# Optimization experiments

Measured on AMD Instinct MI355X. Metric: run time of the kernel, lower is better.

The kernel has to match this reference:

```python
import jax, jax.numpy as jnp
import numpy as np

BIN = 48
CPG = BIN * 3            # 144 hidden channels
SCALE = 2.0 / (BIN - 1)  # quantization step


def _causal_mask(k, include_center):
    # PixelCNN-style raster causal mask for a k x k kernel
    m = np.zeros((k, k), np.float32)
    c = k // 2
    m[:c, :] = 1.0
    m[c, :c] = 1.0
    if include_center:
        m[c, c] = 1.0
    return jnp.asarray(m)

MASK_NC = _causal_mask(5, False)  # first layer: strictly causal (exclude center)
MASK_C = _causal_mask(5, True)    # hidden/final layers: include center


def mconv(x, w, b, mask):
    # masked 5x5 conv, SAME padding, NCHW / OIHW
    y = jax.lax.conv_general_dilated(x, w * mask, (1, 1), 'SAME',
                                     dimension_numbers=('NCHW', 'OIHW', 'NCHW'))
    return y + b[None, :, None, None]


def setup_inputs() -> dict:
    key = jax.random.key(0)
    ks = jax.random.split(key, 8)
    H, W = 256, 512
    std = 0.02
    # quantized code in [-1, 1] on the bin grid, as produced by the decode loop
    lv = jax.random.randint(ks[0], (1, 1, H, W), 0, BIN)
    x = lv.astype(jnp.float32) * SCALE - 1.0
    return {
        'x': x,
        'w0': jax.random.normal(ks[1], (CPG, 1, 5, 5), jnp.float32) * std,
        'b0': jax.random.normal(ks[2], (CPG,), jnp.float32) * std,
        'wr': jax.random.normal(ks[3], (10, CPG, CPG, 5, 5), jnp.float32) * std,
        'br': jax.random.normal(ks[4], (10, CPG), jnp.float32) * std,
        'wf': jax.random.normal(ks[5], (BIN + 1, CPG, 5, 5), jnp.float32) * std,
        'bf': jax.random.normal(ks[6], (BIN + 1,), jnp.float32) * std,
    }


def reference(x, w0, b0, wr, br, wf, bf):
    # causal conv entropy network (CconvDc stack + 5 residual blocks)
    h = jax.nn.relu(mconv(x, w0, b0, MASK_NC))
    for i in range(5):  # EntropyResidualBlockD x5 (fixed small layer loop)
        y = jax.nn.relu(mconv(h, wr[2 * i], br[2 * i], MASK_C))
        y = jax.nn.relu(mconv(y, wr[2 * i + 1], br[2 * i + 1], MASK_C))
        h = h + y
    logits = mconv(h, wf, bf, MASK_C)            # (1, BIN+1, H, W)
    probs = jax.nn.softmax(logits, axis=1)       # per-pixel symbol distribution (EntropyTable input)

    # tail of forward: importance code -> channel mask -> depth-to-space x2
    tcode = jnp.floor((x + 1.0) / SCALE + 1e-5)  # (1,1,H,W) in [0, BIN-1]
    ch = jnp.arange(BIN * 4, dtype=x.dtype)[None, :, None, None]
    tmask = (ch < tcode * 4.0).astype(x.dtype)   # Imp2mask: (1, 4*BIN, H, W)
    N, C, H, W = tmask.shape
    t = tmask.reshape(N, C // 4, 2, 2, H, W)
    t = t.transpose(0, 1, 4, 2, 5, 3).reshape(N, C // 4, 2 * H, 2 * W)  # Dtow(2)
    return probs, t
```

## Files before the change

### kernel.cpp

```cpp
#include <hip/hip_runtime.h>
#include <hip/hip_bf16.h>
#include <stdint.h>

#define H 256
#define W 512
#define NCG 18
#define AW 520
#define AH 258
#define XB 16
#define ROWB (AW*XB)
#define CGB (AH*ROWB)
#define ACTB ((size_t)NCG*(size_t)CGB)
#define KG 236
#define NCHUNK 59
#define CHUNKB 9216
#define WPH_B ((size_t)KG*144*16)
#define WPF_B ((size_t)KG*64*16)

typedef float f32x4 __attribute__((ext_vector_type(4)));
typedef short bf16x8 __attribute__((ext_vector_type(8)));

__device__ __forceinline__ float bf2f(unsigned short u) {
  union { unsigned int i; float f; } v; v.i = ((unsigned int)u) << 16; return v.f;
}
__device__ __forceinline__ unsigned short f2bf(float f) {
  __hip_bfloat16 h = __float2bfloat16(f);
  return __builtin_bit_cast(unsigned short, h);
}
__device__ __forceinline__ void gload_lds16(const void* g, void* l) {
  __builtin_amdgcn_global_load_lds(
      (const __attribute__((address_space(1))) unsigned int*)g,
      (__attribute__((address_space(3))) unsigned int*)l, 16, 0, 0);
}

__global__ void k_pack_h(const float* __restrict__ wr, char* __restrict__ wph) {
  int idx = blockIdx.x * 256 + threadIdx.x;
  if (idx >= 10 * 144 * 144) return;
  int ci = idx % 144; int rem = idx / 144; int co = rem % 144; int layer = rem / 144;
  const float* src = wr + (size_t)((layer * 144 + co) * 144 + ci) * 25;
  unsigned short* dstL = (unsigned short*)(wph + (size_t)layer * WPH_B);
  int cig = ci >> 3, cis = ci & 7;
#pragma unroll
  for (int tap = 0; tap < 13; ++tap) {
    int ky = (tap >= 5) + (tap >= 10);
    int kx = tap - ky * 5;
    dstL[((size_t)(tap * 18 + cig) * 144 + co) * 8 + cis] = f2bf(src[ky * 5 + kx]);
  }
}
__global__ void k_pack_f(const float* __restrict__ wf, char* __restrict__ wpf) {
  int idx = blockIdx.x * 256 + threadIdx.x;
  if (idx >= 49 * 144) return;
  int ci = idx % 144; int co = idx / 144;
  const float* src = wf + (size_t)(co * 144 + ci) * 25;
  unsigned short* dst = (unsigned short*)wpf;
  int cig = ci >> 3, cis = ci & 7;
#pragma unroll
  for (int tap = 0; tap < 13; ++tap) {
    int ky = (tap >= 5) + (tap >= 10);
    int kx = tap - ky * 5;
    dst[((size_t)(tap * 18 + cig) * 64 + co) * 8 + cis] = f2bf(src[ky * 5 + kx]);
  }
}
__global__ void k_biaspad(const float* __restrict__ bf, float* __restrict__ bfp) {
  int i = threadIdx.x;
  bfp[i] = (i < 49) ? bf[i] : -1e30f;
}

__global__ void k_layer0(const float* __restrict__ x, const float* __restrict__ w0,
                         const float* __restrict__ b0, char* __restrict__ act) {
  int i = blockIdx.x * 256 + threadIdx.x;
  int y = i >> 9, xx = i & 511;
  float xv[12];
#pragma unroll
  for (int tp = 0; tp < 12; ++tp) {
    int ky = (tp >= 5) + (tp >= 10);
    int kx = tp - ky * 5;
    int yy = y + ky - 2, xs = xx + kx - 2;
    bool ok = (yy >= 0) && (xs >= 0) && (xs < W);
    xv[tp] = ok ? x[yy * W + xs] : 0.f;
  }
  char* ob = act + (size_t)(y + 2) * ROWB + (size_t)(xx + 2) * XB;
  for (int cg = 0; cg < NCG; ++cg) {
    unsigned int us[4];
#pragma unroll
    for (int h2 = 0; h2 < 4; ++h2) {
      unsigned int lohi = 0;
#pragma unroll
      for (int p = 0; p < 2; ++p) {
        int co = cg * 8 + h2 * 2 + p;
        float a = b0[co];
#pragma unroll
        for (int tp = 0; tp < 12; ++tp) {
          int ky = (tp >= 5) + (tp >= 10);
          int kx = tp - ky * 5;
          a += w0[co * 25 + ky * 5 + kx] * xv[tp];
        }
        a = fmaxf(a, 0.f);
        lohi |= ((unsigned int)f2bf(a)) << (16 * p);
      }
      us[h2] = lohi;
    }
    uint4 v; v.x = us[0]; v.y = us[1]; v.z = us[2]; v.w = us[3];
    *(uint4*)(ob + (size_t)cg * CGB) = v;
  }
}

__global__ __launch_bounds__(256, 2)
void k_conv(const char* __restrict__ in, char* __restrict__ out,
            const char* __restrict__ wp, const float* __restrict__ bias, int res) {
  __shared__ __align__(16) char lA[2][CHUNKB];
  const int tid = threadIdx.x;
  const int wid = tid >> 6, lane = tid & 63;
  const int col = lane & 15, g = lane >> 4;

  int bid = blockIdx.x;
  int xcd = bid & 7, idx = bid >> 3;
  int by = xcd * 8 + (idx >> 3), bx = idx & 7;
  int y = by * 4 + wid, x0 = bx * 64;

  int pxo[4];
#pragma unroll
  for (int t = 0; t < 4; ++t) pxo[t] = (x0 + 16 * t + col) * XB;
  const char* bbase = in + (size_t)y * ROWB;

  f32x4 acc[9][4];
#pragma unroll
  for (int m = 0; m < 9; ++m)
#pragma unroll
    for (int t = 0; t < 4; ++t) acc[m][t] = (f32x4){0.f, 0.f, 0.f, 0.f};

  int ci = g << 3, tap = 0;
  bf16x8 bc[4], bn[4];

  {
    int off = (ci >> 3) * (int)CGB;
#pragma unroll
    for (int t = 0; t < 4; ++t) bc[t] = *(const bf16x8*)(bbase + (size_t)(off + pxo[t]));
  }
  ci += 32; if (ci >= 144) { ci -= 144; ++tap; }

#pragma unroll
  for (int j0 = 0; j0 < 3; ++j0) {
    int j = wid + j0 * 4;
    if (j < 9) gload_lds16(wp + (size_t)j * 1024 + (lane << 4), &lA[0][j * 1024]);
  }
  asm volatile("s_waitcnt vmcnt(0)" ::: "memory");
  __builtin_amdgcn_s_barrier();
  asm volatile("" ::: "memory");

#pragma unroll 1
  for (int c = 0; c < NCHUNK; ++c) {
    const char* ldsp = &lA[c & 1][0];
    if (c < NCHUNK - 1) {
      char* ldsn = &lA[(c & 1) ^ 1][0];
      const char* wsrc = wp + (size_t)(c + 1) * CHUNKB;
#pragma unroll
      for (int j0 = 0; j0 < 3; ++j0) {
        int j = wid + j0 * 4;
        if (j < 9) gload_lds16(wsrc + (size_t)j * 1024 + (lane << 4), ldsn + j * 1024);
      }
      asm volatile("" ::: "memory");
      int ky = (tap >= 5) + (tap >= 10);
      int kx = tap - ky * 5;
      int off = (ci >> 3) * (int)CGB + ky * (int)ROWB + (kx << 4);
#pragma unroll
      for (int t = 0; t < 4; ++t) bn[t] = *(const bf16x8*)(bbase + (size_t)(off + pxo[t]));
      ci += 32; if (ci >= 144) { ci -= 144; ++tap; }
      asm volatile("" ::: "memory");
    }
    const char* abase = ldsp + ((g * 144 + col) << 4);
#pragma unroll
    for (int m = 0; m < 9; ++m) {
      bf16x8 a = *(const bf16x8*)(abase + m * 256);
#pragma unroll
      for (int t = 0; t < 4; ++t)
        acc[m][t] = __builtin_amdgcn_mfma_f32_16x16x32_bf16(a, bc[t], acc[m][t], 0, 0, 0);
    }
    if (c < NCHUNK - 1) {
#pragma unroll
      for (int t = 0; t < 4; ++t) bc[t] = bn[t];
      asm volatile("s_waitcnt vmcnt(4)" ::: "memory");
      __builtin_amdgcn_s_barrier();
      asm volatile("" ::: "memory");
    }
  }

  const int sub = (g & 1) * 8;
#pragma unroll
  for (int m = 0; m < 9; ++m) {
    int co0 = m * 16 + (g << 2);
    f32x4 bv = *(const f32x4*)(bias + co0);
    char* ob = out + (size_t)(co0 >> 3) * CGB + (size_t)(y + 2) * ROWB + sub + 32;
#pragma unroll
    for (int t = 0; t < 4; ++t) {
      char* oa = ob + pxo[t];
      float v0 = fmaxf(acc[m][t][0] + bv[0], 0.f);
      float v1 = fmaxf(acc[m][t][1] + bv[1], 0.f);
      float v2 = fmaxf(acc[m][t][2] + bv[2], 0.f);
      float v3 = fmaxf(acc[m][t][3] + bv[3], 0.f);
      if (res) {
        uint2 old = *(const uint2*)oa;
        v0 += bf2f((unsigned short)(old.x & 0xffff));
        v1 += bf2f((unsigned short)(old.x >> 16));
        v2 += bf2f((unsigned short)(old.y & 0xffff));
        v3 += bf2f((unsigned short)(old.y >> 16));
      }
      uint2 st;
      st.x = (unsigned int)f2bf(v0) | ((unsigned int)f2bf(v1) << 16);
      st.y = (unsigned int)f2bf(v2) | ((unsigned int)f2bf(v3) << 16);
      *(uint2*)oa = st;
    }
  }
}

__global__ __launch_bounds__(256, 2)
void k_convf(const char* __restrict__ in, float* __restrict__ probs,
             const char* __restrict__ wp, const float* __restrict__ bfp) {
  __shared__ __align__(16) char lA[2][4096];
  const int tid = threadIdx.x;
  const int wid = tid >> 6, lane = tid & 63;
  const int col = lane & 15, g = lane >> 4;

  int bid = blockIdx.x;
  int xcd = bid & 7, idx = bid >> 3;
  int by = xcd * 8 + (idx >> 3), bx = idx & 7;
  int y = by * 4 + wid, x0 = bx * 64;

  int pxo[4];
#pragma unroll
  for (int t = 0; t < 4; ++t) pxo[t] = (x0 + 16 * t + col) * XB;
  const char* bbase = in + (size_t)y * ROWB;

  f32x4 acc[4][4];
#pragma unroll
  for (int m = 0; m < 4; ++m)
#pragma unroll
    for (int t = 0; t < 4; ++t) acc[m][t] = (f32x4){0.f, 0.f, 0.f, 0.f};

  int ci = g << 3, tap = 0;
  bf16x8 bc[4], bn[4];
  {
    int off = (ci >> 3) * (int)CGB;
#pragma unroll
    for (int t = 0; t < 4; ++t) bc[t] = *(const bf16x8*)(bbase + (size_t)(off + pxo[t]));
  }
  ci += 32; if (ci >= 144) { ci -= 144; ++tap; }

  if (wid < 4) gload_lds16(wp + (size_t)wid * 1024 + (lane << 4), &lA[0][wid * 1024]);
  asm volatile("s_waitcnt vmcnt(0)" ::: "memory");
  __builtin_amdgcn_s_barrier();
  asm volatile("" ::: "memory");

#pragma unroll 1
  for (int c = 0; c < NCHUNK; ++c) {
    const char* ldsp = &lA[c & 1][0];
    if (c < NCHUNK - 1) {
      char* ldsn = &lA[(c & 1) ^ 1][0];
      const char* wsrc = wp + (size_t)(c + 1) * 4096;
      if (wid < 4) gload_lds16(wsrc + (size_t)wid * 1024 + (lane << 4), ldsn + wid * 1024);
      asm volatile("" ::: "memory");
      int ky = (tap >= 5) + (tap >= 10);
      int kx = tap - ky * 5;
      int off = (ci >> 3) * (int)CGB + ky * (int)ROWB + (kx << 4);
#pragma unroll
      for (int t = 0; t < 4; ++t) bn[t] = *(const bf16x8*)(bbase + (size_t)(off + pxo[t]));
      ci += 32; if (ci >= 144) { ci -= 144; ++tap; }
      asm volatile("" ::: "memory");
    }
    const char* abase = ldsp + ((g * 64 + col) << 4);
#pragma unroll
    for (int m = 0; m < 4; ++m) {
      bf16x8 a = *(const bf16x8*)(abase + m * 256);
#pragma unroll
      for (int t = 0; t < 4; ++t)
        acc[m][t] = __builtin_amdgcn_mfma_f32_16x16x32_bf16(a, bc[t], acc[m][t], 0, 0, 0);
    }
    if (c < NCHUNK - 1) {
#pragma unroll
      for (int t = 0; t < 4; ++t) bc[t] = bn[t];
      asm volatile("s_waitcnt vmcnt(4)" ::: "memory");
      __builtin_amdgcn_s_barrier();
      asm volatile("" ::: "memory");
    }
  }

#pragma unroll
  for (int t = 0; t < 4; ++t) {
    float lg[4][4];
    float mx = -1e30f;
#pragma unroll
    for (int m = 0; m < 4; ++m) {
      f32x4 bv = *(const f32x4*)(bfp + m * 16 + (g << 2));
#pragma unroll
      for (int r = 0; r < 4; ++r) {
        lg[m][r] = acc[m][t][r] + bv[r];
        mx = fmaxf(mx, lg[m][r]);
      }
    }
    mx = fmaxf(mx, __shfl_xor(mx, 16));
    mx = fmaxf(mx, __shfl_xor(mx, 32));
    float s = 0.f;
#pragma unroll
    for (int m = 0; m < 4; ++m)
#pragma unroll
      for (int r = 0; r < 4; ++r) {
        lg[m][r] = __expf(lg[m][r] - mx);
        s += lg[m][r];
      }
    s += __shfl_xor(s, 16);
    s += __shfl_xor(s, 32);
    float inv = 1.f / s;
    int xp = x0 + 16 * t + col;
    float* op = probs + (size_t)y * W + xp;
#pragma unroll
    for (int m = 0; m < 4; ++m)
#pragma unroll
      for (int r = 0; r < 4; ++r) {
        int co = m * 16 + (g << 2) + r;
        if (co < 49) op[(size_t)co * (H * W)] = lg[m][r] * inv;
      }
  }
}

__global__ void k_tmask(const float* __restrict__ x, float* __restrict__ out1) {
  int i = blockIdx.x * 256 + threadIdx.x;
  int yy = i >> 10, xx = i & 1023;
  float xv = x[(yy >> 1) * W + (xx >> 1)];
  float tc = floorf((xv + 1.0f) / (float)(2.0 / 47.0) + 1e-5f);
#pragma unroll 4
  for (int g = 0; g < 48; ++g)
    out1[(size_t)g * (512 * 1024) + i] = ((float)g < tc) ? 1.0f : 0.0f;
}

extern "C" void kernel_launch(void* const* d_in, const int* in_sizes, int n_in,
                              void* d_out, int out_size, void* d_ws, size_t ws_size,
                              hipStream_t stream) {
  const float* x  = (const float*)d_in[0];
  const float* w0 = (const float*)d_in[1];
  const float* b0 = (const float*)d_in[2];
  const float* wr = (const float*)d_in[3];
  const float* br = (const float*)d_in[4];
  const float* wf = (const float*)d_in[5];
  const float* bf = (const float*)d_in[6];

  char* ws   = (char*)d_ws;
  char* actA = ws;
  char* actB = ws + ACTB;
  char* wph  = ws + 2 * ACTB;
  char* wpf  = wph + 10 * WPH_B;
  float* bfp = (float*)(wpf + WPF_B);
  size_t total = 2 * ACTB + 10 * WPH_B + WPF_B + 256;

  hipMemsetAsync(d_ws, 0, total, stream);

  k_pack_h<<<(10 * 144 * 144 + 255) / 256, 256, 0, stream>>>(wr, wph);
  k_pack_f<<<(49 * 144 + 255) / 256, 256, 0, stream>>>(wf, wpf);
  k_biaspad<<<1, 64, 0, stream>>>(bf, bfp);

  k_layer0<<<512, 256, 0, stream>>>(x, w0, b0, actA);

  for (int i = 0; i < 5; ++i) {
    k_conv<<<512, 256, 0, stream>>>(actA, actB, wph + (size_t)(2 * i) * WPH_B,
                                    br + (2 * i) * 144, 0);
    k_conv<<<512, 256, 0, stream>>>(actB, actA, wph + (size_t)(2 * i + 1) * WPH_B,
                                    br + (2 * i + 1) * 144, 1);
  }

  float* probs = (float*)d_out;
  k_convf<<<512, 256, 0, stream>>>(actA, probs, wpf, bfp);
  k_tmask<<<2048, 256, 0, stream>>>(x, probs + (size_t)49 * H * W);
}
```

Before: 902.5 us.

## Zero only activation halos, reorder K-chunks cig-major, unroll double-buffer loop

Replaces the full workspace memset, which cleared both large activation buffers, with a small kernel that zeroes only their padding borders; weights are still memset. Packed weight order changes from tap-major to channel-group-major so each chunk's four groups walk consecutive taps of the same channel group, which may improve cache locality of the activation reads. The main conv loops are unrolled by two with explicit ping-pong register and LDS buffers, removing the per-iteration register copy and conditionals. The risk is that interior halo assumptions are now correct only if every interior pixel is written before it is read.

```diff
diff --git a/kernel.cpp b/kernel.cpp
--- a/kernel.cpp
+++ b/kernel.cpp
@@ -44,7 +44,7 @@
   for (int tap = 0; tap < 13; ++tap) {
     int ky = (tap >= 5) + (tap >= 10);
     int kx = tap - ky * 5;
-    dstL[((size_t)(tap * 18 + cig) * 144 + co) * 8 + cis] = f2bf(src[ky * 5 + kx]);
+    dstL[((size_t)(cig * 13 + tap) * 144 + co) * 8 + cis] = f2bf(src[ky * 5 + kx]);
   }
 }
 __global__ void k_pack_f(const float* __restrict__ wf, char* __restrict__ wpf) {
@@ -58,12 +58,24 @@
   for (int tap = 0; tap < 13; ++tap) {
     int ky = (tap >= 5) + (tap >= 10);
     int kx = tap - ky * 5;
-    dst[((size_t)(tap * 18 + cig) * 64 + co) * 8 + cis] = f2bf(src[ky * 5 + kx]);
+    dst[((size_t)(cig * 13 + tap) * 64 + co) * 8 + cis] = f2bf(src[ky * 5 + kx]);
   }
 }
 __global__ void k_biaspad(const float* __restrict__ bf, float* __restrict__ bfp) {
   int i = threadIdx.x;
   bfp[i] = (i < 49) ? bf[i] : -1e30f;
+}
+
+__global__ void k_zeropad(char* __restrict__ actA, char* __restrict__ actB) {
+  int i = blockIdx.x * 256 + threadIdx.x;
+  if (i >= 2 * 18 * 2064) return;
+  int s = i % 2064; int p = i / 2064; int cig = p % 18; int buf = p / 18;
+  char* base = (buf ? actB : actA) + (size_t)cig * CGB;
+  int row, colpx;
+  if (s < 1040) { row = s / 520; colpx = s - row * 520; }
+  else { int s2 = s - 1040; row = 2 + (s2 >> 2); int m = s2 & 3; colpx = (m < 2) ? m : (512 + m); }
+  uint4 z; z.x = z.y = z.z = z.w = 0u;
+  *(uint4*)(base + (size_t)row * ROWB + (size_t)colpx * 16) = z;
 }
 
 __global__ void k_layer0(const float* __restrict__ x, const float* __restrict__ w0,
@@ -129,61 +141,64 @@
 #pragma unroll
     for (int t = 0; t < 4; ++t) acc[m][t] = (f32x4){0.f, 0.f, 0.f, 0.f};
 
-  int ci = g << 3, tap = 0;
-  bf16x8 bc[4], bn[4];
-
-  {
-    int off = (ci >> 3) * (int)CGB;
-#pragma unroll
-    for (int t = 0; t < 4; ++t) bc[t] = *(const bf16x8*)(bbase + (size_t)(off + pxo[t]));
-  }
-  ci += 32; if (ci >= 144) { ci -= 144; ++tap; }
-
-#pragma unroll
-  for (int j0 = 0; j0 < 3; ++j0) {
-    int j = wid + j0 * 4;
-    if (j < 9) gload_lds16(wp + (size_t)j * 1024 + (lane << 4), &lA[0][j * 1024]);
-  }
+  bf16x8 bA[4], bB[4];
+
+  auto bload = [&](bf16x8 (&dst)[4], int c) __attribute__((always_inline)) {
+    int kg = 4 * c + g;
+    if (kg >= 234) kg = 0;
+    int cig = kg / 13;
+    int tap = kg - cig * 13;
+    int ky = (tap >= 5) + (tap >= 10);
+    int kx = tap - ky * 5;
+    int off = cig * (int)CGB + ky * (int)ROWB + (kx << 4);
+#pragma unroll
+    for (int t = 0; t < 4; ++t) dst[t] = *(const bf16x8*)(bbase + (size_t)(off + pxo[t]));
+  };
+
+  auto stage = [&](char* ldsn, int c) __attribute__((always_inline)) {
+    const char* wsrc = wp + (size_t)c * CHUNKB;
+#pragma unroll
+    for (int j0 = 0; j0 < 3; ++j0) {
+      int j = wid + j0 * 4;
+      if (j < 9) gload_lds16(wsrc + (size_t)j * 1024 + (lane << 4), ldsn + j * 1024);
+    }
+  };
+
+  auto domfma = [&](const char* ldsc, bf16x8 (&bcur)[4]) __attribute__((always_inline)) {
+    const char* abase = ldsc + ((g * 144 + col) << 4);
+#pragma unroll
+    for (int m = 0; m < 9; ++m) {
+      bf16x8 a = *(const bf16x8*)(abase + m * 256);
+#pragma unroll
+      for (int t = 0; t < 4; ++t)
+        acc[m][t] = __builtin_amdgcn_mfma_f32_16x16x32_bf16(a, bcur[t], acc[m][t], 0, 0, 0);
+    }
+  };
+
+  auto phase = [&](const char* ldsc, char* ldsn, bf16x8 (&bcur)[4], bf16x8 (&bnext)[4],
+                   int c) __attribute__((always_inline)) {
+    stage(ldsn, c + 1);
+    asm volatile("" ::: "memory");
+    bload(bnext, c + 1);
+    asm volatile("" ::: "memory");
+    domfma(ldsc, bcur);
+    asm volatile("s_waitcnt vmcnt(4)" ::: "memory");
+    __builtin_amdgcn_s_barrier();
+    asm volatile("" ::: "memory");
+  };
+
+  bload(bA, 0);
+  stage(&lA[0][0], 0);
   asm volatile("s_waitcnt vmcnt(0)" ::: "memory");
   __builtin_amdgcn_s_barrier();
   asm volatile("" ::: "memory");
 
 #pragma unroll 1
-  for (int c = 0; c < NCHUNK; ++c) {
-    const char* ldsp = &lA[c & 1][0];
-    if (c < NCHUNK - 1) {
-      char* ldsn = &lA[(c & 1) ^ 1][0];
-      const char* wsrc = wp + (size_t)(c + 1) * CHUNKB;
-#pragma unroll
-      for (int j0 = 0; j0 < 3; ++j0) {
-        int j = wid + j0 * 4;
-        if (j < 9) gload_lds16(wsrc + (size_t)j * 1024 + (lane << 4), ldsn + j * 1024);
-      }
-      asm volatile("" ::: "memory");
-      int ky = (tap >= 5) + (tap >= 10);
-      int kx = tap - ky * 5;
-      int off = (ci >> 3) * (int)CGB + ky * (int)ROWB + (kx << 4);
-#pragma unroll
-      for (int t = 0; t < 4; ++t) bn[t] = *(const bf16x8*)(bbase + (size_t)(off + pxo[t]));
-      ci += 32; if (ci >= 144) { ci -= 144; ++tap; }
-      asm volatile("" ::: "memory");
-    }
-    const char* abase = ldsp + ((g * 144 + col) << 4);
-#pragma unroll
-    for (int m = 0; m < 9; ++m) {
-      bf16x8 a = *(const bf16x8*)(abase + m * 256);
-#pragma unroll
-      for (int t = 0; t < 4; ++t)
-        acc[m][t] = __builtin_amdgcn_mfma_f32_16x16x32_bf16(a, bc[t], acc[m][t], 0, 0, 0);
-    }
-    if (c < NCHUNK - 1) {
-#pragma unroll
-      for (int t = 0; t < 4; ++t) bc[t] = bn[t];
-      asm volatile("s_waitcnt vmcnt(4)" ::: "memory");
-      __builtin_amdgcn_s_barrier();
-      asm volatile("" ::: "memory");
-    }
-  }
+  for (int c = 0; c < NCHUNK - 1; c += 2) {
+    phase(&lA[0][0], &lA[1][0], bA, bB, c);
+    phase(&lA[1][0], &lA[0][0], bB, bA, c + 1);
+  }
+  domfma(&lA[0][0], bA);
 
   const int sub = (g & 1) * 8;
 #pragma unroll
@@ -237,52 +252,60 @@
 #pragma unroll
     for (int t = 0; t < 4; ++t) acc[m][t] = (f32x4){0.f, 0.f, 0.f, 0.f};
 
-  int ci = g << 3, tap = 0;
-  bf16x8 bc[4], bn[4];
-  {
-    int off = (ci >> 3) * (int)CGB;
-#pragma unroll
-    for (int t = 0; t < 4; ++t) bc[t] = *(const bf16x8*)(bbase + (size_t)(off + pxo[t]));
-  }
-  ci += 32; if (ci >= 144) { ci -= 144; ++tap; }
-
-  if (wid < 4) gload_lds16(wp + (size_t)wid * 1024 + (lane << 4), &lA[0][wid * 1024]);
+  bf16x8 bA[4], bB[4];
+
+  auto bload = [&](bf16x8 (&dst)[4], int c) __attribute__((always_inline)) {
+    int kg = 4 * c + g;
+    if (kg >= 234) kg = 0;
+    int cig = kg / 13;
+    int tap = kg - cig * 13;
+    int ky = (tap >= 5) + (tap >= 10);
+    int kx = tap - ky * 5;
+    int off = cig * (int)CGB + ky * (int)ROWB + (kx << 4);
+#pragma unroll
+    for (int t = 0; t < 4; ++t) dst[t] = *(const bf16x8*)(bbase + (size_t)(off + pxo[t]));
+  };
+
+  auto stage = [&](char* ldsn, int c) __attribute__((always_inline)) {
+    const char* wsrc = wp + (size_t)c * 4096;
+    if (wid < 4) gload_lds16(wsrc + (size_t)wid * 1024 + (lane << 4), ldsn + wid * 1024);
+  };
+
+  auto domfma = [&](const char* ldsc, bf16x8 (&bcur)[4]) __attribute__((always_inline)) {
+    const char* abase = ldsc + ((g * 64 + col) << 4);
+#pragma unroll
+    for (int m = 0; m < 4; ++m) {
+      bf16x8 a = *(const bf16x8*)(abase + m * 256);
+#pragma unroll
+      for (int t = 0; t < 4; ++t)
+        acc[m][t] = __builtin_amdgcn_mfma_f32_16x16x32_bf16(a, bcur[t], acc[m][t], 0, 0, 0);
+    }
+  };
+
+  auto phase = [&](const char* ldsc, char* ldsn, bf16x8 (&bcur)[4], bf16x8 (&bnext)[4],
+                   int c) __attribute__((always_inline)) {
+    stage(ldsn, c + 1);
+    asm volatile("" ::: "memory");
+    bload(bnext, c + 1);
+    asm volatile("" ::: "memory");
+    domfma(ldsc, bcur);
+    asm volatile("s_waitcnt vmcnt(4)" ::: "memory");
+    __builtin_amdgcn_s_barrier();
+    asm volatile("" ::: "memory");
+  };
+
+  bload(bA, 0);
+  stage(&lA[0][0], 0);
   asm volatile("s_waitcnt vmcnt(0)" ::: "memory");
   __builtin_amdgcn_s_barrier();
   asm volatile("" ::: "memory");
 
 #pragma unroll 1
-  for (int c = 0; c < NCHUNK; ++c) {
-    const char* ldsp = &lA[c & 1][0];
-    if (c < NCHUNK - 1) {
-      char* ldsn = &lA[(c & 1) ^ 1][0];
-      const char* wsrc = wp + (size_t)(c + 1) * 4096;
-      if (wid < 4) gload_lds16(wsrc + (size_t)wid * 1024 + (lane << 4), ldsn + wid * 1024);
-      asm volatile("" ::: "memory");
-      int ky = (tap >= 5) + (tap >= 10);
-      int kx = tap - ky * 5;
-      int off = (ci >> 3) * (int)CGB + ky * (int)ROWB + (kx << 4);
-#pragma unroll
-      for (int t = 0; t < 4; ++t) bn[t] = *(const bf16x8*)(bbase + (size_t)(off + pxo[t]));
-      ci += 32; if (ci >= 144) { ci -= 144; ++tap; }
-      asm volatile("" ::: "memory");
-    }
-    const char* abase = ldsp + ((g * 64 + col) << 4);
-#pragma unroll
-    for (int m = 0; m < 4; ++m) {
-      bf16x8 a = *(const bf16x8*)(abase + m * 256);
-#pragma unroll
-      for (int t = 0; t < 4; ++t)
-        acc[m][t] = __builtin_amdgcn_mfma_f32_16x16x32_bf16(a, bc[t], acc[m][t], 0, 0, 0);
-    }
-    if (c < NCHUNK - 1) {
-#pragma unroll
-      for (int t = 0; t < 4; ++t) bc[t] = bn[t];
-      asm volatile("s_waitcnt vmcnt(4)" ::: "memory");
-      __builtin_amdgcn_s_barrier();
-      asm volatile("" ::: "memory");
-    }
-  }
+  for (int c = 0; c < NCHUNK - 1; c += 2) {
+    phase(&lA[0][0], &lA[1][0], bA, bB, c);
+    phase(&lA[1][0], &lA[0][0], bB, bA, c + 1);
+  }
+  domfma(&lA[0][0], bA);
 
 #pragma unroll
   for (int t = 0; t < 4; ++t) {
@@ -349,9 +372,9 @@
   char* wph  = ws + 2 * ACTB;
   char* wpf  = wph + 10 * WPH_B;
   float* bfp = (float*)(wpf + WPF_B);
-  size_t total = 2 * ACTB + 10 * WPH_B + WPF_B + 256;
-
-  hipMemsetAsync(d_ws, 0, total, stream);
+
+  hipMemsetAsync(wph, 0, 10 * WPH_B + WPF_B + 256, stream);
+  k_zeropad<<<(2 * 18 * 2064 + 255) / 256, 256, 0, stream>>>(actA, actB);
 
   k_pack_h<<<(10 * 144 * 144 + 255) / 256, 256, 0, stream>>>(wr, wph);
   k_pack_f<<<(49 * 144 + 255) / 256, 256, 0, stream>>>(wf, wpf);
```

Measured after the change: 744.8 us. 17.5% less time.
